# Kernel optimization log

Hardware: AMD Instinct MI355X
Metric: run time of the kernel (lower is better)

## Reference

```python
import jax, jax.numpy as jnp
import numpy as np

# BlendParams defaults (pytorch3d)
SIGMA = 1e-4
GAMMA = 1e-4
BG_BLUE = 1.0       # background_color = (1,1,1); module returns channel 2
ZNEAR = 1.0
ZFAR = 100.0
EPS = 1e-10

N, H, W, K = 8, 256, 256, 50


def setup_inputs() -> dict:
    key = jax.random.key(0)
    k1, k2, k3 = jax.random.split(key, 3)
    # depth buffer values in [znear, zfar]
    zbuf = jax.random.uniform(k1, (N, H, W, K), dtype=jnp.float32) * (ZFAR - ZNEAR) + ZNEAR
    # signed (squared) pixel-to-edge distances: small magnitudes near 0
    dists = jax.random.normal(k2, (N, H, W, K), dtype=jnp.float32) * 1e-3
    # face indices; -1 marks empty slots (~1/100000 here, plus explicit tail masking)
    pix_to_face = jax.random.randint(k3, (N, H, W, K), -1, 100000, dtype=jnp.int64)
    # make the last few K-slots empty, as a real rasterizer would
    slot = jnp.arange(K)
    pix_to_face = jnp.where(slot < K - 5, pix_to_face, jnp.int64(-1))
    return {"zbuf": zbuf, "dists": dists, "pix_to_face": pix_to_face}


def reference(zbuf, dists, pix_to_face):
    # softmax_rgb_blend with colors == zbuf broadcast over 3 channels;
    # the module returns images[..., 2] (blue channel of the blended RGBA).
    mask = (pix_to_face >= 0).astype(zbuf.dtype)                      # (N,H,W,K)
    prob = jax.nn.sigmoid(-dists / SIGMA) * mask                      # distance sigmoid
    # z-based softmax weights (stabilized by per-pixel max)
    z_inv = (ZFAR - zbuf) / (ZFAR - ZNEAR) * mask                     # (N,H,W,K)
    z_inv_max = jnp.maximum(jnp.max(z_inv, axis=-1, keepdims=True), EPS)
    weights_num = prob * jnp.exp((z_inv - z_inv_max) / GAMMA)         # (N,H,W,K)
    delta = jnp.maximum(jnp.exp((EPS - z_inv_max) / GAMMA), EPS)      # (N,H,W,1)
    denom = jnp.sum(weights_num, axis=-1, keepdims=True) + delta      # (N,H,W,1)
    # weighted color sum; all three channels equal zbuf, take channel 2
    weighted = jnp.sum(weights_num * zbuf, axis=-1, keepdims=True)    # (N,H,W,1)
    blue = (weighted + delta * BG_BLUE) / denom                       # (N,H,W,1)
    return blue[..., 0]                                               # (N,H,W)
```

## Files before the change

### kernel.cpp

```cpp
#include <hip/hip_runtime.h>


constexpr int K       = 50;
constexpr int KP      = 51;
constexpr int PPB     = 128;
constexpr int THREADS = 128;
constexpr int EPB     = PPB * K;
constexpr int F2_PER_THREAD = EPB / 2 / THREADS;

constexpr float SIGMA     = 1e-4f;
constexpr float INV_SIGMA = 1.0f / SIGMA;
constexpr float GAMMA     = 1e-4f;
constexpr float INVG      = 1.0f / GAMMA;
constexpr float ZFAR      = 100.0f;
constexpr float ZRANGE    = 99.0f;
constexpr float INV_ZRANGE= 1.0f / 99.0f;
constexpr float EPS       = 1e-10f;

__global__ __launch_bounds__(THREADS) void soft_depth_kernel(
    const float* __restrict__ zbuf,
    const float* __restrict__ dists,
    const int*   __restrict__ p2f,
    float*       __restrict__ out)
{
    __shared__ float s_z[PPB * KP];
    __shared__ float s_p[PPB * KP];

    const int t = threadIdx.x;
    const size_t base2 = (size_t)blockIdx.x * (EPB / 2);
    const float2* __restrict__ z2 = (const float2*)zbuf  + base2;
    const float2* __restrict__ d2 = (const float2*)dists + base2;
    const int2*   __restrict__ f2 = (const int2*)p2f     + base2;

    #pragma unroll 5
    for (int i = 0; i < F2_PER_THREAD; ++i) {
        const int idx = t + i * THREADS;
        const float2 z = z2[idx];
        const float2 d = d2[idx];
        const int2   f = f2[idx];
        const int e0 = idx * 2;
        const int p  = (int)((unsigned)e0 / (unsigned)K);
        const int k  = e0 - p * K;

        const bool m0 = (f.x >= 0);
        const bool m1 = (f.y >= 0);
        const float zi0 = m0 ? (ZFAR - z.x) * INV_ZRANGE : 0.0f;
        const float zi1 = m1 ? (ZFAR - z.y) * INV_ZRANGE : 0.0f;
        const float pr0 = m0 ? 1.0f / (1.0f + __expf(d.x * INV_SIGMA)) : 0.0f;
        const float pr1 = m1 ? 1.0f / (1.0f + __expf(d.y * INV_SIGMA)) : 0.0f;

        const int a = p * KP + k;
        s_z[a]     = zi0;
        s_z[a + 1] = zi1;
        s_p[a]     = pr0;
        s_p[a + 1] = pr1;
    }
    __syncthreads();

    float m  = EPS;
    float S1 = 0.0f;
    float S2 = 0.0f;
    const int base = t * KP;
    #pragma unroll 10
    for (int k = 0; k < K; ++k) {
        const float z  = s_z[base + k];
        const float pr = s_p[base + k];
        const float mn = fmaxf(m, z);
        const float sc = __expf((m - mn) * INVG);
        const float e  = __expf((z - mn) * INVG);
        const float w  = pr * e;
        const float zb = ZFAR - z * ZRANGE;
        S1 = S1 * sc + w;
        S2 = S2 * sc + w * zb;
        m  = mn;
    }
    const float delta = fmaxf(__expf((EPS - m) * INVG), EPS);
    out[(size_t)blockIdx.x * PPB + t] = (S2 + delta) / (S1 + delta);
}

extern "C" void kernel_launch(void* const* d_in, const int* in_sizes, int n_in,
                              void* d_out, int out_size, void* d_ws, size_t ws_size,
                              hipStream_t stream) {
    const float* zbuf  = (const float*)d_in[0];
    const float* dists = (const float*)d_in[1];
    const int*   p2f   = (const int*)d_in[2];
    float* out = (float*)d_out;

    const int total_elems = in_sizes[0];
    const int blocks = total_elems / EPB;

    soft_depth_kernel<<<dim3(blocks), dim3(THREADS), 0, stream>>>(
        zbuf, dists, p2f, out);
}
```

Measured before the change: 345.5 us.

## Split each pixel across four lanes with register reduction, drop shared memory

Replaces the shared-memory staging plus one-thread-per-pixel online softmax with four lanes per pixel. Each lane loads its strided float2 chunks directly into registers, computes a max, then weighted sums, and combines results with xor shuffles. This removes the LDS round trip, the barrier and the serial rescale exponentials of the online softmax, and raises thread-level parallelism. The cost is strided per-lane loads that may coalesce less well and a divergent tail load on lane 0.

Result: slower. 353.9 us (+2.5%).

```diff
diff --git a/kernel.cpp b/kernel.cpp
--- a/kernel.cpp
+++ b/kernel.cpp
@@ -1,17 +1,13 @@
 #include <hip/hip_runtime.h>
 
 
-constexpr int K       = 50;
-constexpr int KP      = 51;
-constexpr int PPB     = 128;
-constexpr int THREADS = 128;
-constexpr int EPB     = PPB * K;
-constexpr int F2_PER_THREAD = EPB / 2 / THREADS;
+constexpr int THREADS = 256;
+constexpr int LPP     = 4;
+constexpr int PPB     = THREADS / LPP;
+constexpr int NV      = 14;
 
-constexpr float SIGMA     = 1e-4f;
-constexpr float INV_SIGMA = 1.0f / SIGMA;
-constexpr float GAMMA     = 1e-4f;
-constexpr float INVG      = 1.0f / GAMMA;
+constexpr float INV_SIGMA = 1e4f;
+constexpr float INVG      = 1e4f;
 constexpr float ZFAR      = 100.0f;
 constexpr float ZRANGE    = 99.0f;
 constexpr float INV_ZRANGE= 1.0f / 99.0f;
@@ -23,59 +19,75 @@
     const int*   __restrict__ p2f,
     float*       __restrict__ out)
 {
-    __shared__ float s_z[PPB * KP];
-    __shared__ float s_p[PPB * KP];
+    const int t  = threadIdx.x;
+    const int q  = t & (LPP - 1);
+    const size_t pix   = (size_t)blockIdx.x * PPB + (t >> 2);
+    const size_t cbase = pix * 25 + q;
 
-    const int t = threadIdx.x;
-    const size_t base2 = (size_t)blockIdx.x * (EPB / 2);
-    const float2* __restrict__ z2 = (const float2*)zbuf  + base2;
-    const float2* __restrict__ d2 = (const float2*)dists + base2;
-    const int2*   __restrict__ f2 = (const int2*)p2f     + base2;
+    const float2* __restrict__ z2 = (const float2*)zbuf;
+    const float2* __restrict__ d2 = (const float2*)dists;
+    const int2*   __restrict__ f2 = (const int2*)p2f;
 
-    #pragma unroll 5
-    for (int i = 0; i < F2_PER_THREAD; ++i) {
-        const int idx = t + i * THREADS;
-        const float2 z = z2[idx];
-        const float2 d = d2[idx];
-        const int2   f = f2[idx];
-        const int e0 = idx * 2;
-        const int p  = (int)((unsigned)e0 / (unsigned)K);
-        const int k  = e0 - p * K;
+    float zv[NV];
+    float pv[NV];
 
+    #pragma unroll
+    for (int i = 0; i < 6; ++i) {
+        const size_t c = cbase + 4 * i;
+        const float2 z = z2[c];
+        const float2 d = d2[c];
+        const int2   f = f2[c];
         const bool m0 = (f.x >= 0);
         const bool m1 = (f.y >= 0);
-        const float zi0 = m0 ? (ZFAR - z.x) * INV_ZRANGE : 0.0f;
-        const float zi1 = m1 ? (ZFAR - z.y) * INV_ZRANGE : 0.0f;
-        const float pr0 = m0 ? 1.0f / (1.0f + __expf(d.x * INV_SIGMA)) : 0.0f;
-        const float pr1 = m1 ? 1.0f / (1.0f + __expf(d.y * INV_SIGMA)) : 0.0f;
+        zv[2*i]   = m0 ? (ZFAR - z.x) * INV_ZRANGE : 0.0f;
+        zv[2*i+1] = m1 ? (ZFAR - z.y) * INV_ZRANGE : 0.0f;
+        pv[2*i]   = m0 ? 1.0f / (1.0f + __expf(d.x * INV_SIGMA)) : 0.0f;
+        pv[2*i+1] = m1 ? 1.0f / (1.0f + __expf(d.y * INV_SIGMA)) : 0.0f;
+    }
+    if (q == 0) {
+        const size_t c = pix * 25 + 24;
+        const float2 z = z2[c];
+        const float2 d = d2[c];
+        const int2   f = f2[c];
+        const bool m0 = (f.x >= 0);
+        const bool m1 = (f.y >= 0);
+        zv[12] = m0 ? (ZFAR - z.x) * INV_ZRANGE : 0.0f;
+        zv[13] = m1 ? (ZFAR - z.y) * INV_ZRANGE : 0.0f;
+        pv[12] = m0 ? 1.0f / (1.0f + __expf(d.x * INV_SIGMA)) : 0.0f;
+        pv[13] = m1 ? 1.0f / (1.0f + __expf(d.y * INV_SIGMA)) : 0.0f;
+    } else {
+        zv[12] = zv[13] = 0.0f;
+        pv[12] = pv[13] = 0.0f;
+    }
 
-        const int a = p * KP + k;
-        s_z[a]     = zi0;
-        s_z[a + 1] = zi1;
-        s_p[a]     = pr0;
-        s_p[a + 1] = pr1;
+    float m01 = fmaxf(zv[0], zv[1]),   m23 = fmaxf(zv[2], zv[3]);
+    float m45 = fmaxf(zv[4], zv[5]),   m67 = fmaxf(zv[6], zv[7]);
+    float m89 = fmaxf(zv[8], zv[9]),   mab = fmaxf(zv[10], zv[11]);
+    float mcd = fmaxf(zv[12], zv[13]);
+    float m = fmaxf(fmaxf(fmaxf(m01, m23), fmaxf(m45, m67)),
+                    fmaxf(fmaxf(m89, mab), fmaxf(mcd, EPS)));
+    m = fmaxf(m, __shfl_xor(m, 1));
+    m = fmaxf(m, __shfl_xor(m, 2));
+
+    float S1a = 0.0f, S1b = 0.0f, S2a = 0.0f, S2b = 0.0f;
+    #pragma unroll
+    for (int j = 0; j < NV; j += 2) {
+        const float w0 = pv[j]   * __expf((zv[j]   - m) * INVG);
+        const float w1 = pv[j+1] * __expf((zv[j+1] - m) * INVG);
+        S1a += w0;
+        S1b += w1;
+        S2a += w0 * (ZFAR - zv[j]   * ZRANGE);
+        S2b += w1 * (ZFAR - zv[j+1] * ZRANGE);
     }
-    __syncthreads();
+    float S1 = S1a + S1b;
+    float S2 = S2a + S2b;
+    S1 += __shfl_xor(S1, 1);  S1 += __shfl_xor(S1, 2);
+    S2 += __shfl_xor(S2, 1);  S2 += __shfl_xor(S2, 2);
 
-    float m  = EPS;
-    float S1 = 0.0f;
-    float S2 = 0.0f;
-    const int base = t * KP;
-    #pragma unroll 10
-    for (int k = 0; k < K; ++k) {
-        const float z  = s_z[base + k];
-        const float pr = s_p[base + k];
-        const float mn = fmaxf(m, z);
-        const float sc = __expf((m - mn) * INVG);
-        const float e  = __expf((z - mn) * INVG);
-        const float w  = pr * e;
-        const float zb = ZFAR - z * ZRANGE;
-        S1 = S1 * sc + w;
-        S2 = S2 * sc + w * zb;
-        m  = mn;
+    if (q == 0) {
+        const float delta = fmaxf(__expf((EPS - m) * INVG), EPS);
+        out[pix] = (S2 + delta) / (S1 + delta);
     }
-    const float delta = fmaxf(__expf((EPS - m) * INVG), EPS);
-    out[(size_t)blockIdx.x * PPB + t] = (S2 + delta) / (S1 + delta);
 }
 
 extern "C" void kernel_launch(void* const* d_in, const int* in_sizes, int n_in,
@@ -86,8 +98,8 @@
     const int*   p2f   = (const int*)d_in[2];
     float* out = (float*)d_out;
 
-    const int total_elems = in_sizes[0];
-    const int blocks = total_elems / EPB;
+    const int pixels = out_size;
+    const int blocks = pixels / PPB;
 
     soft_depth_kernel<<<dim3(blocks), dim3(THREADS), 0, stream>>>(
         zbuf, dists, p2f, out);
```
